# Optimization experiments

Hardware: AMD Instinct MI355X
Metric: run time of the kernel (lower is better)

Reference implementation:

```python
import jax, jax.numpy as jnp
import numpy as np

F = 6      # num_factors (== nodes per sample)
H = 32     # hidden_dim
B = 65536  # batch of samples (vectorized version of the per-sample Python loop)


def setup_inputs() -> dict:
    key = jax.random.key(0)
    ks = jax.random.split(key, 20)
    p = lambda k, shape: (jax.random.normal(k, shape, dtype=jnp.float32) * 0.1)
    inp = {
        "factors": jax.random.normal(ks[0], (B, F, F), dtype=jnp.float32),
        # CausalStructureLearner.node_encoder: Linear(F, H)
        "Wn": p(ks[1], (F, H)), "bn": p(ks[2], (H,)),
        # edge_predictor: Linear(2H, H) -> ReLU -> Linear(H, 1) -> Sigmoid
        "We1": p(ks[3], (2 * H, H)), "be1": p(ks[4], (H,)),
        "We2": p(ks[5], (H, 1)), "be2": p(ks[6], (1,)),
        # DynamicsPredictor.dynamics_net: F->H->H->F
        "Wd1": p(ks[7], (F, H)), "bd1": p(ks[8], (H,)),
        "Wd2": p(ks[9], (H, H)), "bd2": p(ks[10], (H,)),
        "Wd3": p(ks[11], (H, F)), "bd3": p(ks[12], (F,)),
        # AnomalyScorer.score_net: 3F->32->16->1 -> Sigmoid
        "Ws1": p(ks[13], (3 * F, 32)), "bs1": p(ks[14], (32,)),
        "Ws2": p(ks[15], (32, 16)), "bs2": p(ks[16], (16,)),
        "Ws3": p(ks[17], (16, 1)), "bs3": p(ks[18], (1,)),
    }
    return inp


def reference(factors, Wn, bn, We1, be1, We2, be2,
              Wd1, bd1, Wd2, bd2, Wd3, bd3,
              Ws1, bs1, Ws2, bs2, Ws3, bs3):
    # --- CausalStructureLearner (vectorized pairwise edge scoring) ---
    nf = factors @ Wn + bn                                  # [B, F, H]
    src = jnp.broadcast_to(nf[:, :, None, :], (B, F, F, H))  # node i
    dst = jnp.broadcast_to(nf[:, None, :, :], (B, F, F, H))  # node j
    pair = jnp.concatenate([src, dst], axis=-1)             # [B, F, F, 2H]
    eh = jax.nn.relu(pair @ We1 + be1)                       # [B, F, F, H]
    adj = jax.nn.sigmoid((eh @ We2 + be2)[..., 0])           # [B, F, F]
    adj = adj * (1.0 - jnp.eye(F, dtype=adj.dtype))          # zero diagonal

    # --- DynamicsPredictor: (adj @ factors.T).T == factors @ adj^T ---
    structured = jnp.einsum('bij,bnj->bni', adj, factors)    # [B, F(nodes), F]
    h = jax.nn.relu(structured @ Wd1 + bd1)
    h = jax.nn.relu(h @ Wd2 + bd2)
    pred = h @ Wd3 + bd3                                     # [B, F, F]

    # --- AnomalyScorer ---
    diff = jnp.abs(factors - pred)
    si = jnp.concatenate([factors, pred, diff], axis=-1)     # [B, F, 3F]
    s = jax.nn.relu(si @ Ws1 + bs1)
    s = jax.nn.relu(s @ Ws2 + bs2)
    s = jax.nn.sigmoid(s @ Ws3 + bs3)                        # [B, F, 1]
    scores = jnp.mean(s, axis=(1, 2))                        # [B]

    return adj, pred, scores
```

## Files before the change

### kernel.cpp

```cpp
#include <hip/hip_runtime.h>
#include <math.h>

#define SPB 42
#define NT  256

__device__ __forceinline__ float sigmoidf_(float x) {
    return 1.0f / (1.0f + __expf(-x));
}

__global__ void fold_kernel(const float* __restrict__ Wn,
                            const float* __restrict__ bn,
                            const float* __restrict__ We1,
                            const float* __restrict__ be1,
                            const float* __restrict__ We2,
                            float* __restrict__ rec) {
    int t = threadIdx.x;
    int h = t >> 4, s = t & 15;
    float val = 0.0f;
    if (s < 6) {
        #pragma unroll
        for (int k = 0; k < 32; ++k) val = fmaf(Wn[s*32+k], We1[k*32+h], val);
    } else if (s < 12) {
        int m = s - 6;
        #pragma unroll
        for (int k = 0; k < 32; ++k) val = fmaf(Wn[m*32+k], We1[(32+k)*32+h], val);
    } else if (s == 12) {
        #pragma unroll
        for (int k = 0; k < 32; ++k) val = fmaf(bn[k], We1[k*32+h] + We1[(32+k)*32+h], val);
        val += be1[h];
    } else if (s == 13) {
        val = We2[h];
    }
    rec[t] = val;
}

#define O_REC  0
#define O_WD1  512
#define O_BD1  704
#define O_WD2  736
#define O_BD2  1760
#define O_WD3  1792
#define O_BD3  1984
#define O_WS1  1992
#define O_BS1  2568
#define O_WS2  2600
#define O_BS2  3112
#define O_WS3  3128
#define O_MISC 3144
#define W_TOT  3148

__device__ __forceinline__ void cpy(float* dst, const float* src, int n, int t) {
    for (int i = t; i < n; i += NT) dst[i] = src[i];
}

__global__ __launch_bounds__(NT) void fused_kernel(
        const float* __restrict__ factors,
        const float* __restrict__ rec_g,
        const float* __restrict__ Wd1, const float* __restrict__ bd1,
        const float* __restrict__ Wd2, const float* __restrict__ bd2,
        const float* __restrict__ Wd3, const float* __restrict__ bd3,
        const float* __restrict__ Ws1, const float* __restrict__ bs1,
        const float* __restrict__ Ws2, const float* __restrict__ bs2,
        const float* __restrict__ Ws3, const float* __restrict__ bs3,
        const float* __restrict__ be2,
        float* __restrict__ adj_out,
        float* __restrict__ pred_out,
        float* __restrict__ scores,
        int B) {
    __shared__ float W[W_TOT];
    __shared__ float adj_s[SPB * 36];
    __shared__ float sc_s[SPB * 6];

    const int t = threadIdx.x;
    cpy(W + O_REC, rec_g, 512, t);
    cpy(W + O_WD1, Wd1, 192, t);
    cpy(W + O_BD1, bd1, 32, t);
    cpy(W + O_WD2, Wd2, 1024, t);
    cpy(W + O_BD2, bd2, 32, t);
    cpy(W + O_WD3, Wd3, 192, t);
    if (t < 6)  W[O_BD3 + t] = bd3[t];
    cpy(W + O_WS1, Ws1, 576, t);
    cpy(W + O_BS1, bs1, 32, t);
    cpy(W + O_WS2, Ws2, 512, t);
    cpy(W + O_BS2, bs2, 16, t);
    cpy(W + O_WS3, Ws3, 16, t);
    if (t == 0) { W[O_MISC] = bs3[0]; W[O_MISC + 1] = be2[0]; }
    __syncthreads();

    const int s = t / 6;
    const int n = t - s * 6;
    const int b = blockIdx.x * SPB + s;
    const bool active = (t < SPB * 6) && (b < B);

    float fall[36], fi[6];

    if (active) {
        const float* f = factors + (size_t)b * 36;
        #pragma unroll
        for (int q = 0; q < 9; ++q) {
            float4 v = reinterpret_cast<const float4*>(f)[q];
            fall[q*4+0] = v.x; fall[q*4+1] = v.y; fall[q*4+2] = v.z; fall[q*4+3] = v.w;
        }
        #pragma unroll
        for (int m = 0; m < 6; ++m) fi[m] = f[n*6 + m];

        float acc[6] = {0.f, 0.f, 0.f, 0.f, 0.f, 0.f};
        for (int h = 0; h < 32; ++h) {
            const float* r = &W[O_REC + h * 16];
            float4 r0 = *reinterpret_cast<const float4*>(&r[0]);
            float4 r1 = *reinterpret_cast<const float4*>(&r[4]);
            float4 r2 = *reinterpret_cast<const float4*>(&r[8]);
            float4 r3 = *reinterpret_cast<const float4*>(&r[12]);
            float ra0 = r0.x, ra1 = r0.y, ra2 = r0.z, ra3 = r0.w, ra4 = r1.x, ra5 = r1.y;
            float rb0 = r1.z, rb1 = r1.w, rb2 = r2.x, rb3 = r2.y, rb4 = r2.z, rb5 = r2.w;
            float c0 = r3.x, w2 = r3.y;

            float uh = c0;
            uh = fmaf(fi[0], ra0, uh); uh = fmaf(fi[1], ra1, uh);
            uh = fmaf(fi[2], ra2, uh); uh = fmaf(fi[3], ra3, uh);
            uh = fmaf(fi[4], ra4, uh); uh = fmaf(fi[5], ra5, uh);
            #pragma unroll
            for (int j = 0; j < 6; ++j) {
                float vj;
                vj = fall[j*6+0] * rb0;
                vj = fmaf(fall[j*6+1], rb1, vj);
                vj = fmaf(fall[j*6+2], rb2, vj);
                vj = fmaf(fall[j*6+3], rb3, vj);
                vj = fmaf(fall[j*6+4], rb4, vj);
                vj = fmaf(fall[j*6+5], rb5, vj);
                float e = fmaxf(uh + vj, 0.0f);
                acc[j] = fmaf(e, w2, acc[j]);
            }
        }
        float b2 = W[O_MISC + 1];
        float* ao = adj_out + (size_t)b * 36 + n * 6;
        #pragma unroll
        for (int j = 0; j < 6; ++j) {
            float av = (j == n) ? 0.0f : sigmoidf_(acc[j] + b2);
            adj_s[s * 36 + n * 6 + j] = av;
            ao[j] = av;
        }
    }
    __syncthreads();

    if (active) {
        float adjv[36];
        #pragma unroll
        for (int q = 0; q < 9; ++q) {
            float4 v = *reinterpret_cast<const float4*>(&adj_s[s * 36 + q * 4]);
            adjv[q*4+0] = v.x; adjv[q*4+1] = v.y; adjv[q*4+2] = v.z; adjv[q*4+3] = v.w;
        }
        float st[6];
        #pragma unroll
        for (int i = 0; i < 6; ++i) {
            float v = 0.f;
            #pragma unroll
            for (int j = 0; j < 6; ++j) v = fmaf(adjv[i*6 + j], fi[j], v);
            st[i] = v;
        }

        float h1[32];
        #pragma unroll
        for (int o4 = 0; o4 < 8; ++o4) {
            float4 v = *reinterpret_cast<const float4*>(&W[O_BD1 + o4*4]);
            h1[o4*4+0] = v.x; h1[o4*4+1] = v.y; h1[o4*4+2] = v.z; h1[o4*4+3] = v.w;
        }
        #pragma unroll
        for (int m = 0; m < 6; ++m) {
            float sm = st[m];
            #pragma unroll
            for (int o4 = 0; o4 < 8; ++o4) {
                float4 w = *reinterpret_cast<const float4*>(&W[O_WD1 + m*32 + o4*4]);
                h1[o4*4+0] = fmaf(sm, w.x, h1[o4*4+0]);
                h1[o4*4+1] = fmaf(sm, w.y, h1[o4*4+1]);
                h1[o4*4+2] = fmaf(sm, w.z, h1[o4*4+2]);
                h1[o4*4+3] = fmaf(sm, w.w, h1[o4*4+3]);
            }
        }
        #pragma unroll
        for (int o = 0; o < 32; ++o) h1[o] = fmaxf(h1[o], 0.0f);

        float h2[32];
        #pragma unroll
        for (int o4 = 0; o4 < 8; ++o4) {
            float4 v = *reinterpret_cast<const float4*>(&W[O_BD2 + o4*4]);
            h2[o4*4+0] = v.x; h2[o4*4+1] = v.y; h2[o4*4+2] = v.z; h2[o4*4+3] = v.w;
        }
        #pragma unroll
        for (int k = 0; k < 32; ++k) {
            float hk = h1[k];
            #pragma unroll
            for (int o4 = 0; o4 < 8; ++o4) {
                float4 w = *reinterpret_cast<const float4*>(&W[O_WD2 + k*32 + o4*4]);
                h2[o4*4+0] = fmaf(hk, w.x, h2[o4*4+0]);
                h2[o4*4+1] = fmaf(hk, w.y, h2[o4*4+1]);
                h2[o4*4+2] = fmaf(hk, w.z, h2[o4*4+2]);
                h2[o4*4+3] = fmaf(hk, w.w, h2[o4*4+3]);
            }
        }
        #pragma unroll
        for (int o = 0; o < 32; ++o) h2[o] = fmaxf(h2[o], 0.0f);

        float pr[6];
        #pragma unroll
        for (int j = 0; j < 6; ++j) pr[j] = W[O_BD3 + j];
        #pragma unroll
        for (int k = 0; k < 32; ++k) {
            float hk = h2[k];
            #pragma unroll
            for (int j = 0; j < 6; ++j) pr[j] = fmaf(hk, W[O_WD3 + k*6 + j], pr[j]);
        }
        float* po = pred_out + (size_t)b * 36 + n * 6;
        #pragma unroll
        for (int j = 0; j < 6; ++j) po[j] = pr[j];

        float df[6];
        #pragma unroll
        for (int j = 0; j < 6; ++j) df[j] = fabsf(fi[j] - pr[j]);

        float s1[32];
        #pragma unroll
        for (int o4 = 0; o4 < 8; ++o4) {
            float4 v = *reinterpret_cast<const float4*>(&W[O_BS1 + o4*4]);
            s1[o4*4+0] = v.x; s1[o4*4+1] = v.y; s1[o4*4+2] = v.z; s1[o4*4+3] = v.w;
        }
        #pragma unroll
        for (int m = 0; m < 6; ++m) {
            float a = fi[m], p = pr[m], d = df[m];
            #pragma unroll
            for (int o4 = 0; o4 < 8; ++o4) {
                float4 wa = *reinterpret_cast<const float4*>(&W[O_WS1 + m*32 + o4*4]);
                float4 wp = *reinterpret_cast<const float4*>(&W[O_WS1 + (6+m)*32 + o4*4]);
                float4 wd = *reinterpret_cast<const float4*>(&W[O_WS1 + (12+m)*32 + o4*4]);
                s1[o4*4+0] = fmaf(a, wa.x, fmaf(p, wp.x, fmaf(d, wd.x, s1[o4*4+0])));
                s1[o4*4+1] = fmaf(a, wa.y, fmaf(p, wp.y, fmaf(d, wd.y, s1[o4*4+1])));
                s1[o4*4+2] = fmaf(a, wa.z, fmaf(p, wp.z, fmaf(d, wd.z, s1[o4*4+2])));
                s1[o4*4+3] = fmaf(a, wa.w, fmaf(p, wp.w, fmaf(d, wd.w, s1[o4*4+3])));
            }
        }
        #pragma unroll
        for (int o = 0; o < 32; ++o) s1[o] = fmaxf(s1[o], 0.0f);

        float s2[16];
        #pragma unroll
        for (int o4 = 0; o4 < 4; ++o4) {
            float4 v = *reinterpret_cast<const float4*>(&W[O_BS2 + o4*4]);
            s2[o4*4+0] = v.x; s2[o4*4+1] = v.y; s2[o4*4+2] = v.z; s2[o4*4+3] = v.w;
        }
        #pragma unroll
        for (int k = 0; k < 32; ++k) {
            float sk = s1[k];
            #pragma unroll
            for (int o4 = 0; o4 < 4; ++o4) {
                float4 w = *reinterpret_cast<const float4*>(&W[O_WS2 + k*16 + o4*4]);
                s2[o4*4+0] = fmaf(sk, w.x, s2[o4*4+0]);
                s2[o4*4+1] = fmaf(sk, w.y, s2[o4*4+1]);
                s2[o4*4+2] = fmaf(sk, w.z, s2[o4*4+2]);
                s2[o4*4+3] = fmaf(sk, w.w, s2[o4*4+3]);
            }
        }
        #pragma unroll
        for (int o = 0; o < 16; ++o) s2[o] = fmaxf(s2[o], 0.0f);

        float s3 = W[O_MISC];
        #pragma unroll
        for (int k4 = 0; k4 < 4; ++k4) {
            float4 w = *reinterpret_cast<const float4*>(&W[O_WS3 + k4*4]);
            s3 = fmaf(s2[k4*4+0], w.x, s3);
            s3 = fmaf(s2[k4*4+1], w.y, s3);
            s3 = fmaf(s2[k4*4+2], w.z, s3);
            s3 = fmaf(s2[k4*4+3], w.w, s3);
        }
        sc_s[s * 6 + n] = sigmoidf_(s3);
    }
    __syncthreads();

    if (active && n == 0) {
        float sum = sc_s[s*6+0] + sc_s[s*6+1] + sc_s[s*6+2]
                  + sc_s[s*6+3] + sc_s[s*6+4] + sc_s[s*6+5];
        scores[b] = sum * (1.0f / 6.0f);
    }
}

extern "C" void kernel_launch(void* const* d_in, const int* in_sizes, int n_in,
                              void* d_out, int out_size, void* d_ws, size_t ws_size,
                              hipStream_t stream) {
    const float* factors = (const float*)d_in[0];
    const float* Wn  = (const float*)d_in[1];
    const float* bn  = (const float*)d_in[2];
    const float* We1 = (const float*)d_in[3];
    const float* be1 = (const float*)d_in[4];
    const float* We2 = (const float*)d_in[5];
    const float* be2 = (const float*)d_in[6];
    const float* Wd1 = (const float*)d_in[7];
    const float* bd1 = (const float*)d_in[8];
    const float* Wd2 = (const float*)d_in[9];
    const float* bd2 = (const float*)d_in[10];
    const float* Wd3 = (const float*)d_in[11];
    const float* bd3 = (const float*)d_in[12];
    const float* Ws1 = (const float*)d_in[13];
    const float* bs1 = (const float*)d_in[14];
    const float* Ws2 = (const float*)d_in[15];
    const float* bs2 = (const float*)d_in[16];
    const float* Ws3 = (const float*)d_in[17];
    const float* bs3 = (const float*)d_in[18];

    int B = in_sizes[0] / 36;

    float* adj_out  = (float*)d_out;
    float* pred_out = (float*)d_out + (size_t)B * 36;
    float* scores   = (float*)d_out + (size_t)B * 72;
    float* rec      = (float*)d_ws;

    hipLaunchKernelGGL(fold_kernel, dim3(1), dim3(512), 0, stream,
                       Wn, bn, We1, be1, We2, rec);

    int nblocks = (B + SPB - 1) / SPB;
    hipLaunchKernelGGL(fused_kernel, dim3(nblocks), dim3(NT), 0, stream,
                       factors, rec,
                       Wd1, bd1, Wd2, bd2, Wd3, bd3,
                       Ws1, bs1, Ws2, bs2, Ws3, bs3, be2,
                       adj_out, pred_out, scores, B);
}
```

Before: 164.0 us.

## Pre-pack all weights into one workspace buffer and pipeline LDS weight loads

The fold kernel now packs every weight and bias into one contiguous workspace buffer, with Wd3 transposed. The main kernel loads that buffer with float4 copies instead of many scalar copy loops, and overlaps the factor loads with the shared-memory fill. Its inner loops software-prefetch weight rows two steps ahead in registers. It also pads the adj shared layout, vectorizes the output stores, and runs all threads through the compute paths without divergence checks. The aim is to cut per-block staging cost and LDS latency stalls, at the cost of higher register pressure under launch_bounds(256,2).

```diff
diff --git a/kernel.cpp b/kernel.cpp
--- a/kernel.cpp
+++ b/kernel.cpp
@@ -1,45 +1,15 @@
 #include <hip/hip_runtime.h>
 #include <math.h>
 
+#define NT  256
 #define SPB 42
-#define NT  256
-
-__device__ __forceinline__ float sigmoidf_(float x) {
-    return 1.0f / (1.0f + __expf(-x));
-}
-
-__global__ void fold_kernel(const float* __restrict__ Wn,
-                            const float* __restrict__ bn,
-                            const float* __restrict__ We1,
-                            const float* __restrict__ be1,
-                            const float* __restrict__ We2,
-                            float* __restrict__ rec) {
-    int t = threadIdx.x;
-    int h = t >> 4, s = t & 15;
-    float val = 0.0f;
-    if (s < 6) {
-        #pragma unroll
-        for (int k = 0; k < 32; ++k) val = fmaf(Wn[s*32+k], We1[k*32+h], val);
-    } else if (s < 12) {
-        int m = s - 6;
-        #pragma unroll
-        for (int k = 0; k < 32; ++k) val = fmaf(Wn[m*32+k], We1[(32+k)*32+h], val);
-    } else if (s == 12) {
-        #pragma unroll
-        for (int k = 0; k < 32; ++k) val = fmaf(bn[k], We1[k*32+h] + We1[(32+k)*32+h], val);
-        val += be1[h];
-    } else if (s == 13) {
-        val = We2[h];
-    }
-    rec[t] = val;
-}
 
 #define O_REC  0
 #define O_WD1  512
 #define O_BD1  704
 #define O_WD2  736
 #define O_BD2  1760
-#define O_WD3  1792
+#define O_WD3T 1792
 #define O_BD3  1984
 #define O_WS1  1992
 #define O_BS1  2568
@@ -47,237 +17,353 @@
 #define O_BS2  3112
 #define O_WS3  3128
 #define O_MISC 3144
-#define W_TOT  3148
-
-__device__ __forceinline__ void cpy(float* dst, const float* src, int n, int t) {
-    for (int i = t; i < n; i += NT) dst[i] = src[i];
+#define W_TOT  3152
+
+#define ADJ_STRIDE 52
+
+__device__ __forceinline__ float sigmoidf_(float x) {
+    return 1.0f / (1.0f + __expf(-x));
 }
 
-__global__ __launch_bounds__(NT) void fused_kernel(
-        const float* __restrict__ factors,
-        const float* __restrict__ rec_g,
+__global__ __launch_bounds__(512) void fold_kernel(
+        const float* __restrict__ Wn,  const float* __restrict__ bn,
+        const float* __restrict__ We1, const float* __restrict__ be1,
+        const float* __restrict__ We2, const float* __restrict__ be2,
         const float* __restrict__ Wd1, const float* __restrict__ bd1,
         const float* __restrict__ Wd2, const float* __restrict__ bd2,
         const float* __restrict__ Wd3, const float* __restrict__ bd3,
         const float* __restrict__ Ws1, const float* __restrict__ bs1,
         const float* __restrict__ Ws2, const float* __restrict__ bs2,
         const float* __restrict__ Ws3, const float* __restrict__ bs3,
-        const float* __restrict__ be2,
-        float* __restrict__ adj_out,
-        float* __restrict__ pred_out,
-        float* __restrict__ scores,
-        int B) {
-    __shared__ float W[W_TOT];
-    __shared__ float adj_s[SPB * 36];
+        float* __restrict__ cat) {
+    const int t = threadIdx.x;
+    {
+        const int h = t >> 4, sl = t & 15;
+        float val = 0.0f;
+        if (sl < 6) {
+            #pragma unroll
+            for (int k = 0; k < 32; ++k) val = fmaf(Wn[sl*32+k], We1[k*32+h], val);
+        } else if (sl < 12) {
+            const int m = sl - 6;
+            #pragma unroll
+            for (int k = 0; k < 32; ++k) val = fmaf(Wn[m*32+k], We1[(32+k)*32+h], val);
+        } else if (sl == 12) {
+            #pragma unroll
+            for (int k = 0; k < 32; ++k) val = fmaf(bn[k], We1[k*32+h] + We1[(32+k)*32+h], val);
+            val += be1[h];
+        } else if (sl == 13) {
+            val = We2[h];
+        }
+        cat[t] = val;
+    }
+    for (int i = 512 + t; i < W_TOT; i += 512) {
+        float v = 0.0f;
+        if      (i < O_BD1)  v = Wd1[i - O_WD1];
+        else if (i < O_WD2)  v = bd1[i - O_BD1];
+        else if (i < O_BD2)  v = Wd2[i - O_WD2];
+        else if (i < O_WD3T) v = bd2[i - O_BD2];
+        else if (i < O_BD3)  { int q = i - O_WD3T; v = Wd3[(q & 31) * 6 + (q >> 5)]; }
+        else if (i < O_WS1)  { int q = i - O_BD3; v = (q < 6) ? bd3[q] : 0.0f; }
+        else if (i < O_BS1)  v = Ws1[i - O_WS1];
+        else if (i < O_WS2)  v = bs1[i - O_BS1];
+        else if (i < O_BS2)  v = Ws2[i - O_WS2];
+        else if (i < O_WS3)  v = bs2[i - O_BS2];
+        else if (i < O_MISC) v = Ws3[i - O_WS3];
+        else { int q = i - O_MISC; v = (q == 0) ? bs3[0] : ((q == 1) ? be2[0] : 0.0f); }
+        cat[i] = v;
+    }
+}
+
+__global__ __launch_bounds__(NT, 2) void fused4_kernel(
+        const float* __restrict__ factors, const float* __restrict__ cat,
+        float* __restrict__ adj_out, float* __restrict__ pred_out,
+        float* __restrict__ scores, int B) {
+    __shared__ __align__(16) float Wsh[W_TOT];
+    __shared__ __align__(16) float adj_s[SPB * ADJ_STRIDE];
     __shared__ float sc_s[SPB * 6];
 
     const int t = threadIdx.x;
-    cpy(W + O_REC, rec_g, 512, t);
-    cpy(W + O_WD1, Wd1, 192, t);
-    cpy(W + O_BD1, bd1, 32, t);
-    cpy(W + O_WD2, Wd2, 1024, t);
-    cpy(W + O_BD2, bd2, 32, t);
-    cpy(W + O_WD3, Wd3, 192, t);
-    if (t < 6)  W[O_BD3 + t] = bd3[t];
-    cpy(W + O_WS1, Ws1, 576, t);
-    cpy(W + O_BS1, bs1, 32, t);
-    cpy(W + O_WS2, Ws2, 512, t);
-    cpy(W + O_BS2, bs2, 16, t);
-    cpy(W + O_WS3, Ws3, 16, t);
-    if (t == 0) { W[O_MISC] = bs3[0]; W[O_MISC + 1] = be2[0]; }
-    __syncthreads();
+    #pragma unroll
+    for (int i0 = 0; i0 < W_TOT; i0 += NT * 4) {
+        const int i = i0 + t * 4;
+        if (i < W_TOT)
+            *reinterpret_cast<float4*>(&Wsh[i]) = *reinterpret_cast<const float4*>(&cat[i]);
+    }
 
     const int s = t / 6;
     const int n = t - s * 6;
     const int b = blockIdx.x * SPB + s;
-    const bool active = (t < SPB * 6) && (b < B);
+    const bool act = (t < SPB * 6);
+    const bool bv = act && (b < B);
+    const int sl_ = (s < SPB) ? s : (SPB - 1);
 
     float fall[36], fi[6];
-
-    if (active) {
+    #pragma unroll
+    for (int q = 0; q < 36; ++q) fall[q] = 0.0f;
+    #pragma unroll
+    for (int m = 0; m < 6; ++m) fi[m] = 0.0f;
+    if (bv) {
         const float* f = factors + (size_t)b * 36;
         #pragma unroll
         for (int q = 0; q < 9; ++q) {
-            float4 v = reinterpret_cast<const float4*>(f)[q];
+            const float4 v = reinterpret_cast<const float4*>(f)[q];
             fall[q*4+0] = v.x; fall[q*4+1] = v.y; fall[q*4+2] = v.z; fall[q*4+3] = v.w;
         }
-        #pragma unroll
-        for (int m = 0; m < 6; ++m) fi[m] = f[n*6 + m];
-
-        float acc[6] = {0.f, 0.f, 0.f, 0.f, 0.f, 0.f};
+        const float* fr = f + n * 6;
+        #pragma unroll
+        for (int q = 0; q < 3; ++q) {
+            const float2 v = reinterpret_cast<const float2*>(fr)[q];
+            fi[q*2+0] = v.x; fi[q*2+1] = v.y;
+        }
+    }
+    __syncthreads();
+
+    float av[6];
+    {
+        float acc[6] = {0.f,0.f,0.f,0.f,0.f,0.f};
+        float4 rA0 = *reinterpret_cast<const float4*>(&Wsh[O_REC + 0]);
+        float4 rA1 = *reinterpret_cast<const float4*>(&Wsh[O_REC + 4]);
+        float4 rA2 = *reinterpret_cast<const float4*>(&Wsh[O_REC + 8]);
+        float4 rA3 = *reinterpret_cast<const float4*>(&Wsh[O_REC + 12]);
+        float4 rB0 = *reinterpret_cast<const float4*>(&Wsh[O_REC + 16]);
+        float4 rB1 = *reinterpret_cast<const float4*>(&Wsh[O_REC + 20]);
+        float4 rB2 = *reinterpret_cast<const float4*>(&Wsh[O_REC + 24]);
+        float4 rB3 = *reinterpret_cast<const float4*>(&Wsh[O_REC + 28]);
+        #pragma unroll 4
         for (int h = 0; h < 32; ++h) {
-            const float* r = &W[O_REC + h * 16];
-            float4 r0 = *reinterpret_cast<const float4*>(&r[0]);
-            float4 r1 = *reinterpret_cast<const float4*>(&r[4]);
-            float4 r2 = *reinterpret_cast<const float4*>(&r[8]);
-            float4 r3 = *reinterpret_cast<const float4*>(&r[12]);
-            float ra0 = r0.x, ra1 = r0.y, ra2 = r0.z, ra3 = r0.w, ra4 = r1.x, ra5 = r1.y;
-            float rb0 = r1.z, rb1 = r1.w, rb2 = r2.x, rb3 = r2.y, rb4 = r2.z, rb5 = r2.w;
-            float c0 = r3.x, w2 = r3.y;
-
-            float uh = c0;
-            uh = fmaf(fi[0], ra0, uh); uh = fmaf(fi[1], ra1, uh);
-            uh = fmaf(fi[2], ra2, uh); uh = fmaf(fi[3], ra3, uh);
-            uh = fmaf(fi[4], ra4, uh); uh = fmaf(fi[5], ra5, uh);
+            const int hn = (h + 2 < 32) ? (h + 2) : h;
+            const float4 rC0 = *reinterpret_cast<const float4*>(&Wsh[O_REC + hn*16 + 0]);
+            const float4 rC1 = *reinterpret_cast<const float4*>(&Wsh[O_REC + hn*16 + 4]);
+            const float4 rC2 = *reinterpret_cast<const float4*>(&Wsh[O_REC + hn*16 + 8]);
+            const float4 rC3 = *reinterpret_cast<const float4*>(&Wsh[O_REC + hn*16 + 12]);
+            float uh = rA3.x;
+            uh = fmaf(fi[0], rA0.x, uh); uh = fmaf(fi[1], rA0.y, uh);
+            uh = fmaf(fi[2], rA0.z, uh); uh = fmaf(fi[3], rA0.w, uh);
+            uh = fmaf(fi[4], rA1.x, uh); uh = fmaf(fi[5], rA1.y, uh);
+            const float w2 = rA3.y;
             #pragma unroll
             for (int j = 0; j < 6; ++j) {
-                float vj;
-                vj = fall[j*6+0] * rb0;
-                vj = fmaf(fall[j*6+1], rb1, vj);
-                vj = fmaf(fall[j*6+2], rb2, vj);
-                vj = fmaf(fall[j*6+3], rb3, vj);
-                vj = fmaf(fall[j*6+4], rb4, vj);
-                vj = fmaf(fall[j*6+5], rb5, vj);
-                float e = fmaxf(uh + vj, 0.0f);
-                acc[j] = fmaf(e, w2, acc[j]);
+                float vj =      fall[j*6+0] * rA1.z;
+                vj = fmaf(fall[j*6+1], rA1.w, vj);
+                vj = fmaf(fall[j*6+2], rA2.x, vj);
+                vj = fmaf(fall[j*6+3], rA2.y, vj);
+                vj = fmaf(fall[j*6+4], rA2.z, vj);
+                vj = fmaf(fall[j*6+5], rA2.w, vj);
+                acc[j] = fmaf(fmaxf(uh + vj, 0.0f), w2, acc[j]);
             }
-        }
-        float b2 = W[O_MISC + 1];
+            rA0 = rB0; rA1 = rB1; rA2 = rB2; rA3 = rB3;
+            rB0 = rC0; rB1 = rC1; rB2 = rC2; rB3 = rC3;
+        }
+        const float b2 = Wsh[O_MISC + 1];
+        #pragma unroll
+        for (int j = 0; j < 6; ++j) av[j] = (j == n) ? 0.0f : sigmoidf_(acc[j] + b2);
+    }
+    if (act) {
+        float* as = &adj_s[sl_ * ADJ_STRIDE + n * 8];
+        *reinterpret_cast<float4*>(&as[0]) = make_float4(av[0], av[1], av[2], av[3]);
+        *reinterpret_cast<float2*>(&as[4]) = make_float2(av[4], av[5]);
+    }
+    if (bv) {
         float* ao = adj_out + (size_t)b * 36 + n * 6;
-        #pragma unroll
-        for (int j = 0; j < 6; ++j) {
-            float av = (j == n) ? 0.0f : sigmoidf_(acc[j] + b2);
-            adj_s[s * 36 + n * 6 + j] = av;
-            ao[j] = av;
-        }
+        *reinterpret_cast<float2*>(&ao[0]) = make_float2(av[0], av[1]);
+        *reinterpret_cast<float2*>(&ao[2]) = make_float2(av[2], av[3]);
+        *reinterpret_cast<float2*>(&ao[4]) = make_float2(av[4], av[5]);
     }
     __syncthreads();
 
-    if (active) {
-        float adjv[36];
-        #pragma unroll
-        for (int q = 0; q < 9; ++q) {
-            float4 v = *reinterpret_cast<const float4*>(&adj_s[s * 36 + q * 4]);
-            adjv[q*4+0] = v.x; adjv[q*4+1] = v.y; adjv[q*4+2] = v.z; adjv[q*4+3] = v.w;
-        }
-        float st[6];
+    float st[6];
+    {
+        const float* as = &adj_s[sl_ * ADJ_STRIDE];
         #pragma unroll
         for (int i = 0; i < 6; ++i) {
-            float v = 0.f;
-            #pragma unroll
-            for (int j = 0; j < 6; ++j) v = fmaf(adjv[i*6 + j], fi[j], v);
+            const float4 qa = *reinterpret_cast<const float4*>(&as[i*8]);
+            const float2 qb = *reinterpret_cast<const float2*>(&as[i*8+4]);
+            float v = fi[0] * qa.x;
+            v = fmaf(fi[1], qa.y, v); v = fmaf(fi[2], qa.z, v);
+            v = fmaf(fi[3], qa.w, v); v = fmaf(fi[4], qb.x, v);
+            v = fmaf(fi[5], qb.y, v);
             st[i] = v;
         }
-
-        float h1[32];
+    }
+
+    float h1[32];
+    #pragma unroll
+    for (int o4 = 0; o4 < 8; ++o4) {
+        const float4 v = *reinterpret_cast<const float4*>(&Wsh[O_BD1 + o4*4]);
+        h1[o4*4+0] = v.x; h1[o4*4+1] = v.y; h1[o4*4+2] = v.z; h1[o4*4+3] = v.w;
+    }
+    #pragma unroll
+    for (int m = 0; m < 6; ++m) {
+        const float sm = st[m];
         #pragma unroll
         for (int o4 = 0; o4 < 8; ++o4) {
-            float4 v = *reinterpret_cast<const float4*>(&W[O_BD1 + o4*4]);
-            h1[o4*4+0] = v.x; h1[o4*4+1] = v.y; h1[o4*4+2] = v.z; h1[o4*4+3] = v.w;
-        }
-        #pragma unroll
-        for (int m = 0; m < 6; ++m) {
-            float sm = st[m];
-            #pragma unroll
-            for (int o4 = 0; o4 < 8; ++o4) {
-                float4 w = *reinterpret_cast<const float4*>(&W[O_WD1 + m*32 + o4*4]);
-                h1[o4*4+0] = fmaf(sm, w.x, h1[o4*4+0]);
-                h1[o4*4+1] = fmaf(sm, w.y, h1[o4*4+1]);
-                h1[o4*4+2] = fmaf(sm, w.z, h1[o4*4+2]);
-                h1[o4*4+3] = fmaf(sm, w.w, h1[o4*4+3]);
-            }
-        }
-        #pragma unroll
-        for (int o = 0; o < 32; ++o) h1[o] = fmaxf(h1[o], 0.0f);
-
-        float h2[32];
+            const float4 w = *reinterpret_cast<const float4*>(&Wsh[O_WD1 + m*32 + o4*4]);
+            h1[o4*4+0] = fmaf(sm, w.x, h1[o4*4+0]);
+            h1[o4*4+1] = fmaf(sm, w.y, h1[o4*4+1]);
+            h1[o4*4+2] = fmaf(sm, w.z, h1[o4*4+2]);
+            h1[o4*4+3] = fmaf(sm, w.w, h1[o4*4+3]);
+        }
+    }
+    #pragma unroll
+    for (int o = 0; o < 32; ++o) h1[o] = fmaxf(h1[o], 0.0f);
+
+    float h2[32];
+    #pragma unroll
+    for (int o4 = 0; o4 < 8; ++o4) {
+        const float4 v = *reinterpret_cast<const float4*>(&Wsh[O_BD2 + o4*4]);
+        h2[o4*4+0] = v.x; h2[o4*4+1] = v.y; h2[o4*4+2] = v.z; h2[o4*4+3] = v.w;
+    }
+    #pragma unroll
+    for (int pass = 0; pass < 2; ++pass) {
+        const int ob = O_WD2 + pass * 16;
+        float4 wA0 = *reinterpret_cast<const float4*>(&Wsh[ob + 0]);
+        float4 wA1 = *reinterpret_cast<const float4*>(&Wsh[ob + 4]);
+        float4 wA2 = *reinterpret_cast<const float4*>(&Wsh[ob + 8]);
+        float4 wA3 = *reinterpret_cast<const float4*>(&Wsh[ob + 12]);
+        float4 wB0 = *reinterpret_cast<const float4*>(&Wsh[ob + 32 + 0]);
+        float4 wB1 = *reinterpret_cast<const float4*>(&Wsh[ob + 32 + 4]);
+        float4 wB2 = *reinterpret_cast<const float4*>(&Wsh[ob + 32 + 8]);
+        float4 wB3 = *reinterpret_cast<const float4*>(&Wsh[ob + 32 + 12]);
+        #pragma unroll
+        for (int k = 0; k < 32; ++k) {
+            const int kn = (k + 2 < 32) ? (k + 2) : k;
+            const float4 wC0 = *reinterpret_cast<const float4*>(&Wsh[ob + kn*32 + 0]);
+            const float4 wC1 = *reinterpret_cast<const float4*>(&Wsh[ob + kn*32 + 4]);
+            const float4 wC2 = *reinterpret_cast<const float4*>(&Wsh[ob + kn*32 + 8]);
+            const float4 wC3 = *reinterpret_cast<const float4*>(&Wsh[ob + kn*32 + 12]);
+            const float x = h1[k];
+            h2[pass*16+ 0] = fmaf(x, wA0.x, h2[pass*16+ 0]);
+            h2[pass*16+ 1] = fmaf(x, wA0.y, h2[pass*16+ 1]);
+            h2[pass*16+ 2] = fmaf(x, wA0.z, h2[pass*16+ 2]);
+            h2[pass*16+ 3] = fmaf(x, wA0.w, h2[pass*16+ 3]);
+            h2[pass*16+ 4] = fmaf(x, wA1.x, h2[pass*16+ 4]);
+            h2[pass*16+ 5] = fmaf(x, wA1.y, h2[pass*16+ 5]);
+            h2[pass*16+ 6] = fmaf(x, wA1.z, h2[pass*16+ 6]);
+            h2[pass*16+ 7] = fmaf(x, wA1.w, h2[pass*16+ 7]);
+            h2[pass*16+ 8] = fmaf(x, wA2.x, h2[pass*16+ 8]);
+            h2[pass*16+ 9] = fmaf(x, wA2.y, h2[pass*16+ 9]);
+            h2[pass*16+10] = fmaf(x, wA2.z, h2[pass*16+10]);
+            h2[pass*16+11] = fmaf(x, wA2.w, h2[pass*16+11]);
+            h2[pass*16+12] = fmaf(x, wA3.x, h2[pass*16+12]);
+            h2[pass*16+13] = fmaf(x, wA3.y, h2[pass*16+13]);
+            h2[pass*16+14] = fmaf(x, wA3.z, h2[pass*16+14]);
+            h2[pass*16+15] = fmaf(x, wA3.w, h2[pass*16+15]);
+            wA0 = wB0; wA1 = wB1; wA2 = wB2; wA3 = wB3;
+            wB0 = wC0; wB1 = wC1; wB2 = wC2; wB3 = wC3;
+        }
+    }
+    #pragma unroll
+    for (int o = 0; o < 32; ++o) h2[o] = fmaxf(h2[o], 0.0f);
+
+    float pr[6];
+    #pragma unroll
+    for (int j = 0; j < 6; ++j) {
+        float v = Wsh[O_BD3 + j];
+        #pragma unroll
+        for (int k4 = 0; k4 < 8; ++k4) {
+            const float4 w = *reinterpret_cast<const float4*>(&Wsh[O_WD3T + j*32 + k4*4]);
+            v = fmaf(h2[k4*4+0], w.x, v);
+            v = fmaf(h2[k4*4+1], w.y, v);
+            v = fmaf(h2[k4*4+2], w.z, v);
+            v = fmaf(h2[k4*4+3], w.w, v);
+        }
+        pr[j] = v;
+    }
+    if (bv) {
+        float* po = pred_out + (size_t)b * 36 + n * 6;
+        *reinterpret_cast<float2*>(&po[0]) = make_float2(pr[0], pr[1]);
+        *reinterpret_cast<float2*>(&po[2]) = make_float2(pr[2], pr[3]);
+        *reinterpret_cast<float2*>(&po[4]) = make_float2(pr[4], pr[5]);
+    }
+
+    float df[6];
+    #pragma unroll
+    for (int j = 0; j < 6; ++j) df[j] = fabsf(fi[j] - pr[j]);
+
+    float s1[32];
+    #pragma unroll
+    for (int o4 = 0; o4 < 8; ++o4) {
+        const float4 v = *reinterpret_cast<const float4*>(&Wsh[O_BS1 + o4*4]);
+        s1[o4*4+0] = v.x; s1[o4*4+1] = v.y; s1[o4*4+2] = v.z; s1[o4*4+3] = v.w;
+    }
+    #pragma unroll
+    for (int m = 0; m < 6; ++m) {
+        const float a = fi[m], p = pr[m], d = df[m];
         #pragma unroll
         for (int o4 = 0; o4 < 8; ++o4) {
-            float4 v = *reinterpret_cast<const float4*>(&W[O_BD2 + o4*4]);
-            h2[o4*4+0] = v.x; h2[o4*4+1] = v.y; h2[o4*4+2] = v.z; h2[o4*4+3] = v.w;
-        }
+            const float4 wa = *reinterpret_cast<const float4*>(&Wsh[O_WS1 + m*32 + o4*4]);
+            const float4 wp = *reinterpret_cast<const float4*>(&Wsh[O_WS1 + (6+m)*32 + o4*4]);
+            const float4 wd = *reinterpret_cast<const float4*>(&Wsh[O_WS1 + (12+m)*32 + o4*4]);
+            s1[o4*4+0] = fmaf(a, wa.x, fmaf(p, wp.x, fmaf(d, wd.x, s1[o4*4+0])));
+            s1[o4*4+1] = fmaf(a, wa.y, fmaf(p, wp.y, fmaf(d, wd.y, s1[o4*4+1])));
+            s1[o4*4+2] = fmaf(a, wa.z, fmaf(p, wp.z, fmaf(d, wd.z, s1[o4*4+2])));
+            s1[o4*4+3] = fmaf(a, wa.w, fmaf(p, wp.w, fmaf(d, wd.w, s1[o4*4+3])));
+        }
+    }
+    #pragma unroll
+    for (int o = 0; o < 32; ++o) s1[o] = fmaxf(s1[o], 0.0f);
+
+    float s2v[16];
+    #pragma unroll
+    for (int o4 = 0; o4 < 4; ++o4) {
+        const float4 v = *reinterpret_cast<const float4*>(&Wsh[O_BS2 + o4*4]);
+        s2v[o4*4+0] = v.x; s2v[o4*4+1] = v.y; s2v[o4*4+2] = v.z; s2v[o4*4+3] = v.w;
+    }
+    {
+        float4 wA0 = *reinterpret_cast<const float4*>(&Wsh[O_WS2 + 0]);
+        float4 wA1 = *reinterpret_cast<const float4*>(&Wsh[O_WS2 + 4]);
+        float4 wA2 = *reinterpret_cast<const float4*>(&Wsh[O_WS2 + 8]);
+        float4 wA3 = *reinterpret_cast<const float4*>(&Wsh[O_WS2 + 12]);
+        float4 wB0 = *reinterpret_cast<const float4*>(&Wsh[O_WS2 + 16 + 0]);
+        float4 wB1 = *reinterpret_cast<const float4*>(&Wsh[O_WS2 + 16 + 4]);
+        float4 wB2 = *reinterpret_cast<const float4*>(&Wsh[O_WS2 + 16 + 8]);
+        float4 wB3 = *reinterpret_cast<const float4*>(&Wsh[O_WS2 + 16 + 12]);
         #pragma unroll
         for (int k = 0; k < 32; ++k) {
-            float hk = h1[k];
-            #pragma unroll
-            for (int o4 = 0; o4 < 8; ++o4) {
-                float4 w = *reinterpret_cast<const float4*>(&W[O_WD2 + k*32 + o4*4]);
-                h2[o4*4+0] = fmaf(hk, w.x, h2[o4*4+0]);
-                h2[o4*4+1] = fmaf(hk, w.y, h2[o4*4+1]);
-                h2[o4*4+2] = fmaf(hk, w.z, h2[o4*4+2]);
-                h2[o4*4+3] = fmaf(hk, w.w, h2[o4*4+3]);
-            }
-        }
-        #pragma unroll
-        for (int o = 0; o < 32; ++o) h2[o] = fmaxf(h2[o], 0.0f);
-
-        float pr[6];
-        #pragma unroll
-        for (int j = 0; j < 6; ++j) pr[j] = W[O_BD3 + j];
-        #pragma unroll
-        for (int k = 0; k < 32; ++k) {
-            float hk = h2[k];
-            #pragma unroll
-            for (int j = 0; j < 6; ++j) pr[j] = fmaf(hk, W[O_WD3 + k*6 + j], pr[j]);
-        }
-        float* po = pred_out + (size_t)b * 36 + n * 6;
-        #pragma unroll
-        for (int j = 0; j < 6; ++j) po[j] = pr[j];
-
-        float df[6];
-        #pragma unroll
-        for (int j = 0; j < 6; ++j) df[j] = fabsf(fi[j] - pr[j]);
-
-        float s1[32];
-        #pragma unroll
-        for (int o4 = 0; o4 < 8; ++o4) {
-            float4 v = *reinterpret_cast<const float4*>(&W[O_BS1 + o4*4]);
-            s1[o4*4+0] = v.x; s1[o4*4+1] = v.y; s1[o4*4+2] = v.z; s1[o4*4+3] = v.w;
-        }
-        #pragma unroll
-        for (int m = 0; m < 6; ++m) {
-            float a = fi[m], p = pr[m], d = df[m];
-            #pragma unroll
-            for (int o4 = 0; o4 < 8; ++o4) {
-                float4 wa = *reinterpret_cast<const float4*>(&W[O_WS1 + m*32 + o4*4]);
-                float4 wp = *reinterpret_cast<const float4*>(&W[O_WS1 + (6+m)*32 + o4*4]);
-                float4 wd = *reinterpret_cast<const float4*>(&W[O_WS1 + (12+m)*32 + o4*4]);
-                s1[o4*4+0] = fmaf(a, wa.x, fmaf(p, wp.x, fmaf(d, wd.x, s1[o4*4+0])));
-                s1[o4*4+1] = fmaf(a, wa.y, fmaf(p, wp.y, fmaf(d, wd.y, s1[o4*4+1])));
-                s1[o4*4+2] = fmaf(a, wa.z, fmaf(p, wp.z, fmaf(d, wd.z, s1[o4*4+2])));
-                s1[o4*4+3] = fmaf(a, wa.w, fmaf(p, wp.w, fmaf(d, wd.w, s1[o4*4+3])));
-            }
-        }
-        #pragma unroll
-        for (int o = 0; o < 32; ++o) s1[o] = fmaxf(s1[o], 0.0f);
-
-        float s2[16];
-        #pragma unroll
-        for (int o4 = 0; o4 < 4; ++o4) {
-            float4 v = *reinterpret_cast<const float4*>(&W[O_BS2 + o4*4]);
-            s2[o4*4+0] = v.x; s2[o4*4+1] = v.y; s2[o4*4+2] = v.z; s2[o4*4+3] = v.w;
-        }
-        #pragma unroll
-        for (int k = 0; k < 32; ++k) {
-            float sk = s1[k];
-            #pragma unroll
-            for (int o4 = 0; o4 < 4; ++o4) {
-                float4 w = *reinterpret_cast<const float4*>(&W[O_WS2 + k*16 + o4*4]);
-                s2[o4*4+0] = fmaf(sk, w.x, s2[o4*4+0]);
-                s2[o4*4+1] = fmaf(sk, w.y, s2[o4*4+1]);
-                s2[o4*4+2] = fmaf(sk, w.z, s2[o4*4+2]);
-                s2[o4*4+3] = fmaf(sk, w.w, s2[o4*4+3]);
-            }
-        }
-        #pragma unroll
-        for (int o = 0; o < 16; ++o) s2[o] = fmaxf(s2[o], 0.0f);
-
-        float s3 = W[O_MISC];
-        #pragma unroll
-        for (int k4 = 0; k4 < 4; ++k4) {
-            float4 w = *reinterpret_cast<const float4*>(&W[O_WS3 + k4*4]);
-            s3 = fmaf(s2[k4*4+0], w.x, s3);
-            s3 = fmaf(s2[k4*4+1], w.y, s3);
-            s3 = fmaf(s2[k4*4+2], w.z, s3);
-            s3 = fmaf(s2[k4*4+3], w.w, s3);
-        }
-        sc_s[s * 6 + n] = sigmoidf_(s3);
-    }
+            const int kn = (k + 2 < 32) ? (k + 2) : k;
+            const float4 wC0 = *reinterpret_cast<const float4*>(&Wsh[O_WS2 + kn*16 + 0]);
+            const float4 wC1 = *reinterpret_cast<const float4*>(&Wsh[O_WS2 + kn*16 + 4]);
+            const float4 wC2 = *reinterpret_cast<const float4*>(&Wsh[O_WS2 + kn*16 + 8]);
+            const float4 wC3 = *reinterpret_cast<const float4*>(&Wsh[O_WS2 + kn*16 + 12]);
+            const float x = s1[k];
+            s2v[ 0] = fmaf(x, wA0.x, s2v[ 0]);
+            s2v[ 1] = fmaf(x, wA0.y, s2v[ 1]);
+            s2v[ 2] = fmaf(x, wA0.z, s2v[ 2]);
+            s2v[ 3] = fmaf(x, wA0.w, s2v[ 3]);
+            s2v[ 4] = fmaf(x, wA1.x, s2v[ 4]);
+            s2v[ 5] = fmaf(x, wA1.y, s2v[ 5]);
+            s2v[ 6] = fmaf(x, wA1.z, s2v[ 6]);
+            s2v[ 7] = fmaf(x, wA1.w, s2v[ 7]);
+            s2v[ 8] = fmaf(x, wA2.x, s2v[ 8]);
+            s2v[ 9] = fmaf(x, wA2.y, s2v[ 9]);
+            s2v[10] = fmaf(x, wA2.z, s2v[10]);
+            s2v[11] = fmaf(x, wA2.w, s2v[11]);
+            s2v[12] = fmaf(x, wA3.x, s2v[12]);
+            s2v[13] = fmaf(x, wA3.y, s2v[13]);
+            s2v[14] = fmaf(x, wA3.z, s2v[14]);
+            s2v[15] = fmaf(x, wA3.w, s2v[15]);
+            wA0 = wB0; wA1 = wB1; wA2 = wB2; wA3 = wB3;
+            wB0 = wC0; wB1 = wC1; wB2 = wC2; wB3 = wC3;
+        }
+    }
+    #pragma unroll
+    for (int o = 0; o < 16; ++o) s2v[o] = fmaxf(s2v[o], 0.0f);
+
+    float s3 = Wsh[O_MISC];
+    #pragma unroll
+    for (int k4 = 0; k4 < 4; ++k4) {
+        const float4 w = *reinterpret_cast<const float4*>(&Wsh[O_WS3 + k4*4]);
+        s3 = fmaf(s2v[k4*4+0], w.x, s3);
+        s3 = fmaf(s2v[k4*4+1], w.y, s3);
+        s3 = fmaf(s2v[k4*4+2], w.z, s3);
+        s3 = fmaf(s2v[k4*4+3], w.w, s3);
+    }
+    if (act) sc_s[sl_ * 6 + n] = sigmoidf_(s3);
     __syncthreads();
 
-    if (active && n == 0) {
-        float sum = sc_s[s*6+0] + sc_s[s*6+1] + sc_s[s*6+2]
-                  + sc_s[s*6+3] + sc_s[s*6+4] + sc_s[s*6+5];
+    if (bv && n == 0) {
+        const float sum = sc_s[sl_*6+0] + sc_s[sl_*6+1] + sc_s[sl_*6+2]
+                        + sc_s[sl_*6+3] + sc_s[sl_*6+4] + sc_s[sl_*6+5];
         scores[b] = sum * (1.0f / 6.0f);
     }
 }
@@ -305,20 +391,19 @@
     const float* Ws3 = (const float*)d_in[17];
     const float* bs3 = (const float*)d_in[18];
 
-    int B = in_sizes[0] / 36;
+    const int B = in_sizes[0] / 36;
 
     float* adj_out  = (float*)d_out;
     float* pred_out = (float*)d_out + (size_t)B * 36;
     float* scores   = (float*)d_out + (size_t)B * 72;
-    float* rec      = (float*)d_ws;
+    float* cat      = (float*)d_ws;
 
     hipLaunchKernelGGL(fold_kernel, dim3(1), dim3(512), 0, stream,
-                       Wn, bn, We1, be1, We2, rec);
-
-    int nblocks = (B + SPB - 1) / SPB;
-    hipLaunchKernelGGL(fused_kernel, dim3(nblocks), dim3(NT), 0, stream,
-                       factors, rec,
+                       Wn, bn, We1, be1, We2, be2,
                        Wd1, bd1, Wd2, bd2, Wd3, bd3,
-                       Ws1, bs1, Ws2, bs2, Ws3, bs3, be2,
-                       adj_out, pred_out, scores, B);
+                       Ws1, bs1, Ws2, bs2, Ws3, bs3, cat);
+
+    const int nblocks = (B + SPB - 1) / SPB;
+    hipLaunchKernelGGL(fused4_kernel, dim3(nblocks), dim3(NT), 0, stream,
+                       factors, cat, adj_out, pred_out, scores, B);
 }
```

New measurement: 160.7 us. 1.02x faster.
